# Kernel tuning notes

Measured on AMD Instinct MI355X. Metric: run time of the kernel, lower is better.

The kernel has to match this reference:

```python
import jax, jax.numpy as jnp
import numpy as np

N, E, B = 50000, 800000, 50
IN_DIM, HID_DIM, OUT_DIM, HEADS = 13, 64, 64, 4
LN_EPS = 1e-5


def _layer_norm(h, g, b):
    mu = jnp.mean(h, axis=-1, keepdims=True)
    var = jnp.mean((h - mu) ** 2, axis=-1, keepdims=True)
    return g * (h - mu) / jnp.sqrt(var + LN_EPS) + b


def _qkv_gat_layer(x, src, dst, Wq, Wk, Wv, Wr, g, b, n_heads, num_nodes):
    """Multi-head QKV-GAT: segment-softmax attention over incoming edges,
    residual (projected if dims differ) + LayerNorm."""
    d_tot = Wq.shape[1]
    dh = d_tot // n_heads
    q = (x @ Wq).reshape(num_nodes, n_heads, dh)
    k = (x @ Wk).reshape(num_nodes, n_heads, dh)
    v = (x @ Wv).reshape(num_nodes, n_heads, dh)
    # edge scores: q[dst] . k[src] / sqrt(dh)   -> [E, H]
    scores = jnp.sum(q[dst] * k[src], axis=-1) * (1.0 / np.sqrt(dh))
    m = jax.ops.segment_max(scores, dst, num_segments=num_nodes)  # [N, H]
    m = jnp.where(jnp.isfinite(m), m, 0.0)  # guard nodes with no in-edges
    ex = jnp.exp(scores - m[dst])                                  # [E, H]
    denom = jax.ops.segment_sum(ex, dst, num_segments=num_nodes)  # [N, H]
    alpha = ex / (denom[dst] + 1e-16)                              # [E, H]
    agg = jax.ops.segment_sum(alpha[:, :, None] * v[src], dst, num_segments=num_nodes)
    out = agg.reshape(num_nodes, d_tot)
    res = x @ Wr if Wr is not None else x
    return _layer_norm(out + res, g, b)


def setup_inputs() -> dict:
    key = jax.random.key(0)
    ks = jax.random.split(key, 16)
    s = 0.1
    nodes = jax.random.normal(ks[0], (N, IN_DIM), jnp.float32)
    edge_index = jnp.stack([
        jax.random.randint(ks[1], (E,), 0, N),
        jax.random.randint(ks[2], (E,), 0, N),
    ]).astype(jnp.int32)
    batch_ptr = jnp.arange(B + 1, dtype=jnp.int32) * (N // B)  # 50 graphs x 1000 nodes
    p = lambda i, sh: jax.random.normal(ks[i], sh, jnp.float32) * s
    return {
        "nodes": nodes, "edge_index": edge_index, "batch_ptr": batch_ptr,
        "Wq1": p(3, (IN_DIM, HID_DIM)), "Wk1": p(4, (IN_DIM, HID_DIM)),
        "Wv1": p(5, (IN_DIM, HID_DIM)), "Wr1": p(6, (IN_DIM, HID_DIM)),
        "g1": jnp.ones((HID_DIM,), jnp.float32), "b1": jnp.zeros((HID_DIM,), jnp.float32),
        "Wq2": p(7, (HID_DIM, OUT_DIM)), "Wk2": p(8, (HID_DIM, OUT_DIM)),
        "Wv2": p(9, (HID_DIM, OUT_DIM)),
        "g2": jnp.ones((OUT_DIM,), jnp.float32), "b2": jnp.zeros((OUT_DIM,), jnp.float32),
    }


def reference(nodes, edge_index, batch_ptr, Wq1, Wk1, Wv1, Wr1, g1, b1,
              Wq2, Wk2, Wv2, g2, b2):
    src, dst = edge_index[0], edge_index[1]
    num_nodes = nodes.shape[0]
    H1 = _qkv_gat_layer(nodes, src, dst, Wq1, Wk1, Wv1, Wr1, g1, b1, HEADS, num_nodes)
    H2 = _qkv_gat_layer(H1, src, dst, Wq2, Wk2, Wv2, None, g2, b2, HEADS, num_nodes)
    # per-graph mean pooling (replaces the Python loop in _pool_mean)
    seg = jnp.searchsorted(batch_ptr, jnp.arange(num_nodes, dtype=batch_ptr.dtype), side="right") - 1
    counts = (batch_ptr[1:] - batch_ptr[:-1]).astype(H2.dtype)
    Q = jax.ops.segment_sum(H2, seg, num_segments=batch_ptr.shape[0] - 1) / counts[:, None]
    return (H2, Q)
```

## Files before the change

kernel.cpp:

```cpp
#include <hip/hip_runtime.h>
#include <hip/hip_fp16.h>
#include <math.h>
#include <stdint.h>

#define LN_EPS 1e-5f

typedef _Float16 f16x8 __attribute__((ext_vector_type(8)));
typedef _Float16 f16x2 __attribute__((ext_vector_type(2)));
typedef float f32x4 __attribute__((ext_vector_type(4)));


__global__ void k_zero(int* __restrict__ counts, int N, float* __restrict__ Q, int BQ) {
  int i = blockIdx.x * 256 + threadIdx.x;
  int total = N + BQ;
  for (; i < total; i += gridDim.x * 256) {
    if (i < N) counts[i] = 0;
    else Q[i - N] = 0.f;
  }
}


__global__ void k_count(const int* __restrict__ dstA, int E, int NREG,
                        int* __restrict__ counts) {
  int region = blockIdx.x & 7;
  if (region >= NREG) return;
  int e = (blockIdx.x >> 3) * 256 + threadIdx.x;
  if (e < E) {
    int d = dstA[e];
    if ((d >> 13) == region) atomicAdd(&counts[d], 1);
  }
}

__global__ void k_scan1(const int* __restrict__ counts, int N,
                        int* __restrict__ offsets, int* __restrict__ blockSums) {
  __shared__ int sh[256];
  int t = threadIdx.x;
  int i = blockIdx.x * 256 + t;
  int v = (i < N) ? counts[i] : 0;
  sh[t] = v;
  __syncthreads();
  for (int off = 1; off < 256; off <<= 1) {
    int x = (t >= off) ? sh[t - off] : 0;
    __syncthreads();
    sh[t] += x;
    __syncthreads();
  }
  if (i < N) offsets[i] = sh[t] - v;
  if (t == 255) blockSums[blockIdx.x] = sh[t];
}

__global__ void k_scan3(int* __restrict__ offsets, int* __restrict__ cursor,
                        const int* __restrict__ blockSums, int N, int E, int NB) {
  __shared__ int sh[256];
  int t = threadIdx.x;
  int bid = blockIdx.x;
  int v = (t < NB && t < bid) ? blockSums[t] : 0;
  sh[t] = v;
  __syncthreads();
  for (int off = 128; off >= 1; off >>= 1) {
    if (t < off) sh[t] += sh[t + off];
    __syncthreads();
  }
  int prefix = sh[0];
  int i = bid * 256 + t;
  if (i < N) {
    int o = offsets[i] + prefix;
    offsets[i] = o;
    cursor[i] = o;
  }
  if (i == 0) offsets[N] = E;
}

__global__ void k_scatter(const int* __restrict__ srcA, const int* __restrict__ dstA,
                          int E, int NREG,
                          int* __restrict__ cursor, int* __restrict__ csr_src) {
  int region = blockIdx.x & 7;
  if (region >= NREG) return;
  int e = (blockIdx.x >> 3) * 256 + threadIdx.x;
  if (e < E) {
    int d = dstA[e];
    if ((d >> 13) == region) {
      int pos = atomicAdd(&cursor[d], 1);
      csr_src[pos] = srcA[e];
    }
  }
}


__global__ void k_proj1(const float* __restrict__ x, const float* __restrict__ Wk,
                        const float* __restrict__ Wv, const float* __restrict__ Wq,
                        const float* __restrict__ Wr, int N,
                        __half* __restrict__ kvh, __half* __restrict__ qh,
                        float* __restrict__ rb) {
  int t = blockIdx.x * blockDim.x + threadIdx.x;
  int n = t >> 6, j = t & 63;
  if (n >= N) return;
  const float* xr = x + (size_t)n * 13;
  float ak = 0.f, av = 0.f, aq = 0.f, ar = 0.f;
#pragma unroll
  for (int i = 0; i < 13; ++i) {
    float xv = xr[i];
    ak = fmaf(xv, Wk[i * 64 + j], ak);
    av = fmaf(xv, Wv[i * 64 + j], av);
    aq = fmaf(xv, Wq[i * 64 + j], aq);
    ar = fmaf(xv, Wr[i * 64 + j], ar);
  }
  __half* row = kvh + (size_t)n * 128;
  int base = (j >> 2) * 8 + (j & 3);
  row[base] = __float2half(ak);
  row[base + 4] = __float2half(av);
  qh[t] = __float2half(aq * 0.25f);
  rb[t] = ar;
}

__global__ void __launch_bounds__(256) k_proj2m(
    const __half* __restrict__ H1h,
    const float* __restrict__ Wk, const float* __restrict__ Wv,
    const float* __restrict__ Wq, int N,
    __half* __restrict__ kvh, __half* __restrict__ qh) {
  int lane = threadIdx.x & 63;
  int wid = threadIdx.x >> 6;
  int col = lane & 15;
  int kgrp = lane >> 4;
  f16x8 bk[2][4], bv[2][4], bq[2][4];
#pragma unroll
  for (int ct = 0; ct < 4; ++ct) {
    int c = ct * 16 + col;
#pragma unroll
    for (int kh = 0; kh < 2; ++kh) {
      int k0 = kh * 32 + kgrp * 8;
      f16x8 fk, fv, fq;
#pragma unroll
      for (int i = 0; i < 8; ++i) {
        fk[i] = (_Float16)Wk[(k0 + i) * 64 + c];
        fv[i] = (_Float16)Wv[(k0 + i) * 64 + c];
        fq[i] = (_Float16)(Wq[(k0 + i) * 64 + c] * 0.25f);
      }
      bk[kh][ct] = fk; bv[kh][ct] = fv; bq[kh][ct] = fq;
    }
  }
  int nTiles = (N + 15) >> 4;
  f32x4 zero = {0.f, 0.f, 0.f, 0.f};
  for (int t = blockIdx.x * 4 + wid; t < nTiles; t += gridDim.x * 4) {
    int n0 = t << 4;
    const f16x8* arow = (const f16x8*)(H1h + ((size_t)n0 + col) * 64);
    f16x8 a0 = arow[kgrp];
    f16x8 a1 = arow[4 + kgrp];
#pragma unroll
    for (int ct = 0; ct < 4; ++ct) {
      f32x4 ck = __builtin_amdgcn_mfma_f32_16x16x32_f16(a0, bk[0][ct], zero, 0, 0, 0);
      ck = __builtin_amdgcn_mfma_f32_16x16x32_f16(a1, bk[1][ct], ck, 0, 0, 0);
      f32x4 cv = __builtin_amdgcn_mfma_f32_16x16x32_f16(a0, bv[0][ct], zero, 0, 0, 0);
      cv = __builtin_amdgcn_mfma_f32_16x16x32_f16(a1, bv[1][ct], cv, 0, 0, 0);
      f32x4 cq = __builtin_amdgcn_mfma_f32_16x16x32_f16(a0, bq[0][ct], zero, 0, 0, 0);
      cq = __builtin_amdgcn_mfma_f32_16x16x32_f16(a1, bq[1][ct], cq, 0, 0, 0);
#pragma unroll
      for (int r = 0; r < 4; ++r) {
        int node = n0 + kgrp * 4 + r;
        if (node < N) {
          size_t rowo = (size_t)node * 128 + (ct * 4 + (col >> 2)) * 8 + (col & 3);
          kvh[rowo] = __float2half(ck[r]);
          kvh[rowo + 4] = __float2half(cv[r]);
          qh[(size_t)node * 64 + ct * 16 + col] = __float2half(cq[r]);
        }
      }
    }
  }
}


__device__ __forceinline__ float dot4h(unsigned int k01, unsigned int k23,
                                       unsigned int q01, unsigned int q23) {
#if __has_builtin(__builtin_amdgcn_fdot2)
  float p = __builtin_amdgcn_fdot2(__builtin_bit_cast(f16x2, k01),
                                   __builtin_bit_cast(f16x2, q01), 0.f, false);
  return __builtin_amdgcn_fdot2(__builtin_bit_cast(f16x2, k23),
                                __builtin_bit_cast(f16x2, q23), p, false);
#else
  float2 ka = __half22float2(*(const __half2*)&k01);
  float2 kb = __half22float2(*(const __half2*)&k23);
  float2 qa = __half22float2(*(const __half2*)&q01);
  float2 qb = __half22float2(*(const __half2*)&q23);
  return ka.x * qa.x + ka.y * qa.y + kb.x * qb.x + kb.y * qb.y;
#endif
}

__device__ __forceinline__ void edge_body(uint4 w, bool vf, uint2 qw,
                                          float& denom, float4& acc) {
  float p = dot4h(w.x, w.y, qw.x, qw.y);
  p += __shfl_xor(p, 1, 64);
  p += __shfl_xor(p, 2, 64);
  float ex = vf ? __expf(p) : 0.f;
  float2 v01 = __half22float2(*(const __half2*)&w.z);
  float2 v23 = __half22float2(*(const __half2*)&w.w);
  denom += ex;
  acc.x = fmaf(ex, v01.x, acc.x);
  acc.y = fmaf(ex, v01.y, acc.y);
  acc.z = fmaf(ex, v23.x, acc.z);
  acc.w = fmaf(ex, v23.y, acc.w);
}

template <int NS>
__device__ __forceinline__ void edge_batch(const uint4* __restrict__ kvh4,
                                           const int* __restrict__ csr_src,
                                           int e0, int base, int deg,
                                           int grp, int sub, uint2 qw,
                                           float& denom, float4& acc) {
  uint4 w[NS];
  bool vf[NS];
#pragma unroll
  for (int s = 0; s < NS; ++s) {
    int idx = base + s * 4 + grp;
    vf[s] = idx < deg;
    int sv = vf[s] ? csr_src[e0 + idx] : 0;
    w[s] = kvh4[(size_t)sv * 16 + sub];
  }
#pragma unroll
  for (int s = 0; s < NS; ++s) edge_body(w[s], vf[s], qw, denom, acc);
}

__device__ __forceinline__ void edge_loop_h(const uint4* __restrict__ kvh4,
                                            const int* __restrict__ csr_src,
                                            int e0, int deg, int lane, uint2 qw,
                                            float& denom, float4& acc) {
  int grp = lane >> 4;
  int sub = lane & 15;
  if (deg <= 16) {
    edge_batch<4>(kvh4, csr_src, e0, 0, deg, grp, sub, qw, denom, acc);
  } else if (deg <= 32) {
    edge_batch<8>(kvh4, csr_src, e0, 0, deg, grp, sub, qw, denom, acc);
  } else {
    for (int base = 0; base < deg; base += 32)
      edge_batch<8>(kvh4, csr_src, e0, base, deg, grp, sub, qw, denom, acc);
  }
#pragma unroll
  for (int off = 16; off <= 32; off <<= 1) {
    acc.x += __shfl_xor(acc.x, off, 64);
    acc.y += __shfl_xor(acc.y, off, 64);
    acc.z += __shfl_xor(acc.z, off, 64);
    acc.w += __shfl_xor(acc.w, off, 64);
    denom += __shfl_xor(denom, off, 64);
  }
}

__device__ __forceinline__ float4 ln_compute(float4 out4, float4 r4,
                                             const float* __restrict__ g,
                                             const float* __restrict__ b, int lane) {
  float4 h;
  h.x = out4.x + r4.x; h.y = out4.y + r4.y; h.z = out4.z + r4.z; h.w = out4.w + r4.w;
  float s = (h.x + h.y) + (h.z + h.w);
#pragma unroll
  for (int off = 1; off <= 8; off <<= 1) s += __shfl_xor(s, off, 64);
  float mu = s * 0.015625f;
  float4 d;
  d.x = h.x - mu; d.y = h.y - mu; d.z = h.z - mu; d.w = h.w - mu;
  float v = (d.x * d.x + d.y * d.y) + (d.z * d.z + d.w * d.w);
#pragma unroll
  for (int off = 1; off <= 8; off <<= 1) v += __shfl_xor(v, off, 64);
  float rs = rsqrtf(v * 0.015625f + LN_EPS);
  float4 o = make_float4(0.f, 0.f, 0.f, 0.f);
  if (lane < 16) {
    int c = lane * 4;
    float4 g4 = *(const float4*)&g[c];
    float4 b4 = *(const float4*)&b[c];
    o.x = fmaf(g4.x, d.x * rs, b4.x);
    o.y = fmaf(g4.y, d.y * rs, b4.y);
    o.z = fmaf(g4.z, d.z * rs, b4.z);
    o.w = fmaf(g4.w, d.w * rs, b4.w);
  }
  return o;
}


__global__ void __launch_bounds__(256) k_gat1(
    const __half* __restrict__ qh, const float* __restrict__ rb,
    const uint4* __restrict__ kvh4,
    const int* __restrict__ offsets, const int* __restrict__ csr_src,
    const float* __restrict__ g, const float* __restrict__ b,
    int N, __half* __restrict__ H1h) {
  int wid = threadIdx.x >> 6, lane = threadIdx.x & 63;
  int n = blockIdx.x * 4 + wid;
  if (n >= N) return;
  int sub = lane & 15;
  uint2 qw = *(const uint2*)&qh[(size_t)n * 64 + sub * 4];
  float4 r4 = *(const float4*)&rb[(size_t)n * 64 + sub * 4];
  int e0 = offsets[n];
  int deg = offsets[n + 1] - e0;
  float denom = 0.f;
  float4 acc = make_float4(0.f, 0.f, 0.f, 0.f);
  edge_loop_h(kvh4, csr_src, e0, deg, lane, qw, denom, acc);
  float inv = 1.0f / (denom + 1e-16f);
  float4 out4 = make_float4(acc.x * inv, acc.y * inv, acc.z * inv, acc.w * inv);
  float4 o = ln_compute(out4, r4, g, b, lane);
  if (lane < 16) {
    __half2 p0 = __floats2half2_rn(o.x, o.y);
    __half2 p1 = __floats2half2_rn(o.z, o.w);
    uint2 pw;
    pw.x = *(unsigned int*)&p0;
    pw.y = *(unsigned int*)&p1;
    *(uint2*)&H1h[(size_t)n * 64 + lane * 4] = pw;
  }
}

__global__ void __launch_bounds__(256) k_gat2(
    const __half* __restrict__ H1h, const __half* __restrict__ qh,
    const uint4* __restrict__ kvh4,
    const int* __restrict__ offsets, const int* __restrict__ csr_src,
    const float* __restrict__ g, const float* __restrict__ b,
    int N, float* __restrict__ H2) {
  int wid = threadIdx.x >> 6, lane = threadIdx.x & 63;
  int n = blockIdx.x * 4 + wid;
  if (n >= N) return;
  int sub = lane & 15;
  uint2 qw = *(const uint2*)&qh[(size_t)n * 64 + sub * 4];
  uint2 rw = *(const uint2*)&H1h[(size_t)n * 64 + sub * 4];
  const __half2* rp = (const __half2*)&rw;
  float2 ra = __half22float2(rp[0]), rb2 = __half22float2(rp[1]);
  float4 r4 = make_float4(ra.x, ra.y, rb2.x, rb2.y);
  int e0 = offsets[n];
  int deg = offsets[n + 1] - e0;
  float denom = 0.f;
  float4 acc = make_float4(0.f, 0.f, 0.f, 0.f);
  edge_loop_h(kvh4, csr_src, e0, deg, lane, qw, denom, acc);
  float inv = 1.0f / (denom + 1e-16f);
  float4 out4 = make_float4(acc.x * inv, acc.y * inv, acc.z * inv, acc.w * inv);
  float4 o = ln_compute(out4, r4, g, b, lane);
  if (lane < 16) *(float4*)&H2[(size_t)n * 64 + lane * 4] = o;
}


#define POOL_CHUNKS 16

__global__ void __launch_bounds__(256) k_pool(const float* __restrict__ H2,
                                              const int* __restrict__ ptr,
                                              float* __restrict__ Q) {
  __shared__ float sh[4 * 64];
  int gI = blockIdx.x / POOL_CHUNKS;
  int c  = blockIdx.x % POOL_CHUNKS;
  int start = ptr[gI], end = ptr[gI + 1];
  int cnt = end - start;
  int per = (cnt + POOL_CHUNKS - 1) / POOL_CHUNKS;
  int s = start + c * per;
  int e = min(s + per, end);
  int wid = threadIdx.x >> 6, lane = threadIdx.x & 63;
  float acc = 0.f;
  for (int n = s + wid; n < e; n += 4) acc += H2[(size_t)n * 64 + lane];
  sh[wid * 64 + lane] = acc;
  __syncthreads();
  if (wid == 0) {
    float v = sh[lane] + sh[64 + lane] + sh[128 + lane] + sh[192 + lane];
    atomicAdd(&Q[(size_t)gI * 64 + lane], v / (float)cnt);
  }
}


extern "C" void kernel_launch(void* const* d_in, const int* in_sizes, int n_in,
                              void* d_out, int out_size, void* d_ws, size_t ws_size,
                              hipStream_t stream) {
  const float* nodes = (const float*)d_in[0];
  const int* eidx    = (const int*)d_in[1];
  const int* bptr    = (const int*)d_in[2];
  const float* Wq1 = (const float*)d_in[3];
  const float* Wk1 = (const float*)d_in[4];
  const float* Wv1 = (const float*)d_in[5];
  const float* Wr1 = (const float*)d_in[6];
  const float* g1  = (const float*)d_in[7];
  const float* b1  = (const float*)d_in[8];
  const float* Wq2 = (const float*)d_in[9];
  const float* Wk2 = (const float*)d_in[10];
  const float* Wv2 = (const float*)d_in[11];
  const float* g2  = (const float*)d_in[12];
  const float* b2  = (const float*)d_in[13];

  const int N = in_sizes[0] / 13;
  const int E = in_sizes[1] / 2;
  const int B = in_sizes[2] - 1;
  const int* srcA = eidx;
  const int* dstA = eidx + E;

  char* w = (char*)d_ws;
  int* counts    = (int*)w; w += (size_t)N * 4;
  int* offsets   = (int*)w; w += (size_t)(N + 1) * 4;
  int* blockSums = (int*)w; w += 256 * 4;
  int* csr_src   = (int*)w; w += (size_t)E * 4;
  w = (char*)(((uintptr_t)w + 255) & ~(uintptr_t)255);
  __half* kvh = (__half*)w; w += (size_t)N * 128 * 2;
  __half* qh  = (__half*)w; w += (size_t)N * 64 * 2;
  float*  rb  = (float*)w;  w += (size_t)N * 64 * 4;
  __half* H1h = (__half*)rb;

  float* H2 = (float*)d_out;
  float* Q  = H2 + (size_t)N * 64;

  const int NB = (N + 255) / 256;
  const int EB = (E + 255) / 256;
  const int GB = (N + 3) / 4;
  const int NREG = ((N - 1) >> 13) + 1;

  k_zero<<<256, 256, 0, stream>>>(counts, N, Q, B * 64);
  k_count<<<EB * 8, 256, 0, stream>>>(dstA, E, NREG, counts);
  k_scan1<<<NB, 256, 0, stream>>>(counts, N, offsets, blockSums);
  k_scan3<<<NB, 256, 0, stream>>>(offsets, counts, blockSums, N, E, NB);
  k_scatter<<<EB * 8, 256, 0, stream>>>(srcA, dstA, E, NREG, counts, csr_src);

  k_proj1<<<(N * 64 + 255) / 256, 256, 0, stream>>>(nodes, Wk1, Wv1, Wq1, Wr1, N,
                                                    kvh, qh, rb);
  k_gat1<<<GB, 256, 0, stream>>>(qh, rb, (const uint4*)kvh, offsets, csr_src,
                                 g1, b1, N, H1h);
  k_proj2m<<<392, 256, 0, stream>>>(H1h, Wk2, Wv2, Wq2, N, kvh, qh);
  k_gat2<<<GB, 256, 0, stream>>>(H1h, qh, (const uint4*)kvh, offsets, csr_src,
                                 g2, b2, N, H2);
  k_pool<<<B * POOL_CHUNKS, 256, 0, stream>>>(H2, bptr, Q);
}
```

Before: 198.3 us.

## Bind CSR build regions to XCC via hardware id and atomic chunk tickets

The count and scatter kernels now read the hardware XCC id and have each block process only the destination region matching its XCC. Blocks on each XCC pull edge chunks from a per-region atomic ticket counter. Previously regions were assigned by blockIdx modulo 8, which relies on round-robin block dispatch. The intent is to keep each region's atomics inside one XCC's L2 and avoid cross-die coherence traffic. This adds ticket atomics and a dependence on the XCC id register, and only 7 of the 8 XCCs get work.

```diff
diff --git a/kernel.cpp b/kernel.cpp
--- a/kernel.cpp
+++ b/kernel.cpp
@@ -9,9 +9,17 @@
 typedef _Float16 f16x2 __attribute__((ext_vector_type(2)));
 typedef float f32x4 __attribute__((ext_vector_type(4)));
 
-
-__global__ void k_zero(int* __restrict__ counts, int N, float* __restrict__ Q, int BQ) {
+__device__ __forceinline__ int xcc_id() {
+  unsigned v;
+  asm volatile("s_getreg_b32 %0, hwreg(HW_REG_XCC_ID)" : "=s"(v));
+  return (int)(v & 7);
+}
+
+
+__global__ void k_zero(int* __restrict__ counts, int N, float* __restrict__ Q, int BQ,
+                       int* __restrict__ tickets) {
   int i = blockIdx.x * 256 + threadIdx.x;
+  if (blockIdx.x == 0) tickets[threadIdx.x] = 0;
   int total = N + BQ;
   for (; i < total; i += gridDim.x * 256) {
     if (i < N) counts[i] = 0;
@@ -20,14 +28,50 @@
 }
 
 
-__global__ void k_count(const int* __restrict__ dstA, int E, int NREG,
-                        int* __restrict__ counts) {
-  int region = blockIdx.x & 7;
-  if (region >= NREG) return;
-  int e = (blockIdx.x >> 3) * 256 + threadIdx.x;
-  if (e < E) {
-    int d = dstA[e];
-    if ((d >> 13) == region) atomicAdd(&counts[d], 1);
+#define CHUNK 2048
+
+__global__ void __launch_bounds__(256) k_count(
+    const int* __restrict__ dstA, int E, int NREG,
+    int* __restrict__ tickets, int* __restrict__ counts) {
+  int r = xcc_id();
+  if (r >= NREG) return;
+  __shared__ int sChunk;
+  int nCh = (E + CHUNK - 1) / CHUNK;
+  for (;;) {
+    if (threadIdx.x == 0) sChunk = atomicAdd(&tickets[r * 16], 1);
+    __syncthreads();
+    int c = sChunk;
+    __syncthreads();
+    if (c >= nCh) break;
+    int end = min(c * CHUNK + CHUNK, E);
+    for (int e = c * CHUNK + threadIdx.x; e < end; e += 256) {
+      int d = dstA[e];
+      if ((d >> 13) == r) atomicAdd(&counts[d], 1);
+    }
+  }
+}
+
+__global__ void __launch_bounds__(256) k_scatter(
+    const int* __restrict__ srcA, const int* __restrict__ dstA, int E, int NREG,
+    int* __restrict__ tickets, int* __restrict__ cursor, int* __restrict__ csr_src) {
+  int r = xcc_id();
+  if (r >= NREG) return;
+  __shared__ int sChunk;
+  int nCh = (E + CHUNK - 1) / CHUNK;
+  for (;;) {
+    if (threadIdx.x == 0) sChunk = atomicAdd(&tickets[128 + r * 16], 1);
+    __syncthreads();
+    int c = sChunk;
+    __syncthreads();
+    if (c >= nCh) break;
+    int end = min(c * CHUNK + CHUNK, E);
+    for (int e = c * CHUNK + threadIdx.x; e < end; e += 256) {
+      int d = dstA[e];
+      if ((d >> 13) == r) {
+        int pos = atomicAdd(&cursor[d], 1);
+        csr_src[pos] = srcA[e];
+      }
+    }
   }
 }
 
@@ -69,21 +113,6 @@
     cursor[i] = o;
   }
   if (i == 0) offsets[N] = E;
-}
-
-__global__ void k_scatter(const int* __restrict__ srcA, const int* __restrict__ dstA,
-                          int E, int NREG,
-                          int* __restrict__ cursor, int* __restrict__ csr_src) {
-  int region = blockIdx.x & 7;
-  if (region >= NREG) return;
-  int e = (blockIdx.x >> 3) * 256 + threadIdx.x;
-  if (e < E) {
-    int d = dstA[e];
-    if ((d >> 13) == region) {
-      int pos = atomicAdd(&cursor[d], 1);
-      csr_src[pos] = srcA[e];
-    }
-  }
 }
 
 
@@ -379,6 +408,7 @@
   const int* dstA = eidx + E;
 
   char* w = (char*)d_ws;
+  int* tickets   = (int*)w; w += 256 * 4;
   int* counts    = (int*)w; w += (size_t)N * 4;
   int* offsets   = (int*)w; w += (size_t)(N + 1) * 4;
   int* blockSums = (int*)w; w += 256 * 4;
@@ -393,15 +423,14 @@
   float* Q  = H2 + (size_t)N * 64;
 
   const int NB = (N + 255) / 256;
-  const int EB = (E + 255) / 256;
   const int GB = (N + 3) / 4;
   const int NREG = ((N - 1) >> 13) + 1;
 
-  k_zero<<<256, 256, 0, stream>>>(counts, N, Q, B * 64);
-  k_count<<<EB * 8, 256, 0, stream>>>(dstA, E, NREG, counts);
+  k_zero<<<256, 256, 0, stream>>>(counts, N, Q, B * 64, tickets);
+  k_count<<<2048, 256, 0, stream>>>(dstA, E, NREG, tickets, counts);
   k_scan1<<<NB, 256, 0, stream>>>(counts, N, offsets, blockSums);
   k_scan3<<<NB, 256, 0, stream>>>(offsets, counts, blockSums, N, E, NB);
-  k_scatter<<<EB * 8, 256, 0, stream>>>(srcA, dstA, E, NREG, counts, csr_src);
+  k_scatter<<<2048, 256, 0, stream>>>(srcA, dstA, E, NREG, tickets, counts, csr_src);
 
   k_proj1<<<(N * 64 + 255) / 256, 256, 0, stream>>>(nodes, Wk1, Wv1, Wq1, Wr1, N,
                                                     kvh, qh, rb);
```

Measured after the change: 218.7 us. +10.3%, slower.
